# Performance work log

Measured on AMD Instinct MI355X. Metric: run time of the kernel, lower is better.

The kernel has to match this reference:

```python
import jax, jax.numpy as jnp
import numpy as np

B = 4; IN_CH = 256; HEAD_CH = 64; NUM_CLS = 3; H = 128; W = 128
NH = 4; KEY = 16; VAL = 16; OUT_CH = 2
VX = 0.1 * 8; VY = 0.1 * 8  # voxel_size[:2] * out_size_factor
DW = 1.6; DL = 3.9; STRIDE = 1
C_CTR = (HEAD_CH + 2 + NUM_CLS) * 9      # 621
C_COR = (HEAD_CH + 2 + NUM_CLS * 4) * 8  # 624
C_FG = (HEAD_CH + 2 + NUM_CLS) * 9       # 621


def _sampler_points():
    offs = np.arange(-STRIDE, STRIDE + 1, STRIDE, dtype=np.float32)
    oy, ox = np.meshgrid(offs, offs, indexing='ij')
    ctr = np.stack([ox, oy], 0).reshape(2, 9)  # pixel offsets
    cx = np.array([-DW/2, -DW/2, DW/2, DW/2, DL/2, -DL/2, DL/2, -DL/2], np.float32) / VX
    cy = np.array([DL/2, -DL/2, DL/2, -DL/2, -DW/2, -DW/2, DW/2, DW/2], np.float32) / VY
    # faithful to torch: stack(dim=1) -> [8,2] then .view(2,8) (row-major reinterpret)
    cor = np.stack([cx, cy], 1).reshape(2, 8)
    r = max(DW, DL)
    fx = np.array([-r/3, -r/3, -r/3, 0, 0, 0, r/3, r/3, r/3], np.float32) / VX
    fy = np.array([-r/3, 0, r/3, -r/3, 0, r/3, -r/3, 0, r/3], np.float32) / VY
    fg = np.stack([fx, fy], 1).reshape(2, 9)
    return jnp.asarray(ctr), jnp.asarray(cor), jnp.asarray(fg)


def _raw_grid():
    gx = jnp.arange(W, dtype=jnp.float32) + 0.5
    gy = jnp.arange(H, dtype=jnp.float32) + 0.5
    return jnp.stack([jnp.broadcast_to(gx[None, :], (H, W)),
                      jnp.broadcast_to(gy[:, None], (H, W))], 0)  # [2,H,W]


def _conv3x3(x, w, b):
    y = jax.lax.conv_general_dilated(x, w, (1, 1), 'SAME',
                                     dimension_numbers=('NCHW', 'OIHW', 'NCHW'))
    return y + b[None, :, None, None]


def _cbr3(x, w, b, s, t):  # conv3x3 + inference-mode BN (folded scale/shift) + relu
    return jax.nn.relu(_conv3x3(x, w, b) * s[None, :, None, None] + t[None, :, None, None])


def _cbr1(x, w, b, s, t):  # per-head 1x1 conv + BN + relu, w: [NH,O,C], x: [B,C,H,W]
    y = jnp.einsum('noc,bchw->nbohw', w, x) + b[:, None, :, None, None]
    return jax.nn.relu(y * s[:, None, :, None, None] + t[:, None, :, None, None])


def _sample(feats, grids):
    # feats [B,C,H,W]; grids [2,n,H,W] pixel coords. Matches F.grid_sample
    # (bilinear, zeros padding, align_corners=False): sample at pixel coord g-0.5.
    n = grids.shape[1]
    geo = jnp.stack([grids[0] / W, grids[1] / H], 0)  # recover_coords, [2,n,H,W]
    gx, gy = grids[0] - 0.5, grids[1] - 0.5
    x0f = jnp.floor(gx); y0f = jnp.floor(gy)
    dx, dy = gx - x0f, gy - y0f
    x0 = x0f.astype(jnp.int32); y0 = y0f.astype(jnp.int32)
    flat = feats.reshape(B, -1, H * W)

    def gather(xc, yc, wgt):
        valid = ((xc >= 0) & (xc < W) & (yc >= 0) & (yc < H)).astype(feats.dtype) * wgt
        idx = jnp.clip(yc, 0, H - 1) * W + jnp.clip(xc, 0, W - 1)
        v = jnp.take(flat, idx.reshape(-1), axis=2).reshape(B, -1, n, H, W)
        return v * valid[None, None]

    s = (gather(x0, y0, (1 - dx) * (1 - dy)) + gather(x0 + 1, y0, dx * (1 - dy))
         + gather(x0, y0 + 1, (1 - dx) * dy) + gather(x0 + 1, y0 + 1, dx * dy))
    geo_b = jnp.broadcast_to(geo[None], (B,) + geo.shape)
    out = jnp.concatenate([s, geo_b], axis=1)  # [B,C+2,n,H,W]
    return out.reshape(B, -1, H, W)           # channel index = c*n + p, as torch .view


def _forward(base_feats, cc_w, cc_b, cc_s, cc_t, ch_w, ch_b,
             oc_w, oc_b, oc_s, oc_t, oh_w, oh_b,
             fc_w, fc_b, fc_s, fc_t, fh_w, fh_b,
             q_w, q_b, q_s, q_t,
             ck_w, ck_b, ck_s, ck_t, cv_w, cv_b, cv_s, cv_t,
             kk_w, kk_b, kk_s, kk_t, kv_w, kv_b, kv_s, kv_t,
             fk_w, fk_b, fk_s, fk_t, fv_w, fv_b, fv_s, fv_t,
             p1_w, p1_b, p1_s, p1_t, p2_w, p2_b):
    center_feat = _cbr3(base_feats, cc_w, cc_b, cc_s, cc_t)
    center_map = _conv3x3(center_feat, ch_w, ch_b)
    corner_feat = _cbr3(base_feats, oc_w, oc_b, oc_s, oc_t)
    corner_map = _conv3x3(corner_feat, oh_w, oh_b)
    fg_feat = _cbr3(base_feats, fc_w, fc_b, fc_s, fc_t)
    fg_map = _conv3x3(fg_feat, fh_w, fh_b)

    ctr_pts, cor_pts, fg_pts = _sampler_points()
    raw = _raw_grid()
    g_ctr = raw[:, None] + ctr_pts[:, :, None, None]  # [2,9,H,W]
    g_cor = raw[:, None] + cor_pts[:, :, None, None]  # [2,8,H,W]
    g_fg = raw[:, None] + fg_pts[:, :, None, None]    # [2,9,H,W]

    cs = _sample(jnp.concatenate([center_feat, center_map], 1), g_ctr)  # [B,621,H,W]
    os_ = _sample(jnp.concatenate([corner_feat, corner_map], 1), g_cor)  # [B,624,H,W]
    fs = _sample(jnp.concatenate([fg_feat, fg_map], 1), g_fg)            # [B,621,H,W]

    q = _cbr1(base_feats, q_w, q_b, q_s, q_t)  # [NH,B,KEY,H,W]
    ck = _cbr1(cs, ck_w, ck_b, ck_s, ck_t); cv = _cbr1(cs, cv_w, cv_b, cv_s, cv_t)
    ok = _cbr1(os_, kk_w, kk_b, kk_s, kk_t); ov = _cbr1(os_, kv_w, kv_b, kv_s, kv_t)
    fk = _cbr1(fs, fk_w, fk_b, fk_s, fk_t); fv = _cbr1(fs, fv_w, fv_b, fv_s, fv_t)

    logits = jnp.stack([(q * ck).sum(2), (q * ok).sum(2), (q * fk).sum(2)], axis=2)  # [NH,B,3,H,W]
    attw = jax.nn.softmax(logits, axis=2)
    vals = jnp.stack([cv, ov, fv], axis=2)          # [NH,B,3,VAL,H,W]
    att = (attw[:, :, :, None] * vals).sum(2)       # [NH,B,VAL,H,W]

    # predict: 1x1 conv over cat([base_feats, att]) + BN + relu, then 1x1 to out_ch
    h1 = (jnp.einsum('noc,bchw->nbohw', p1_w[:, :, :IN_CH], base_feats)
          + jnp.einsum('nov,nbvhw->nbohw', p1_w[:, :, IN_CH:], att)
          + p1_b[:, None, :, None, None])
    h1 = jax.nn.relu(h1 * p1_s[:, None, :, None, None] + p1_t[:, None, :, None, None])
    pred = jnp.einsum('npo,nbohw->nbphw', p2_w, h1) + p2_b[:, None, :, None, None]
    heads = jnp.moveaxis(pred, 0, 1).reshape(B, NH * OUT_CH, H, W)
    return jnp.concatenate([center_map, corner_map, fg_map, heads], axis=1)  # [B,26,H,W]


def setup_inputs() -> dict:
    ks = iter(jax.random.split(jax.random.key(0), 80))

    def rn(shape, s=0.05):
        return jax.random.normal(next(ks), shape, jnp.float32) * s

    d = {"base_feats": jax.random.normal(next(ks), (B, IN_CH, H, W), jnp.float32)}
    for conv, head, hc in (("cc", "ch", NUM_CLS), ("oc", "oh", NUM_CLS * 4), ("fc", "fh", NUM_CLS)):
        d[conv + "_w"] = rn((HEAD_CH, IN_CH, 3, 3)); d[conv + "_b"] = rn((HEAD_CH,))
        d[conv + "_s"] = 1.0 + rn((HEAD_CH,)); d[conv + "_t"] = rn((HEAD_CH,))
        d[head + "_w"] = rn((hc, HEAD_CH, 3, 3)); d[head + "_b"] = jnp.full((hc,), -2.19, jnp.float32)
    d["q_w"] = rn((NH, KEY, IN_CH)); d["q_b"] = rn((NH, KEY))
    d["q_s"] = 1.0 + rn((NH, KEY)); d["q_t"] = rn((NH, KEY))
    for name, cin, cout in (("ck", C_CTR, KEY), ("cv", C_CTR, VAL), ("kk", C_COR, KEY),
                            ("kv", C_COR, VAL), ("fk", C_FG, KEY), ("fv", C_FG, VAL)):
        d[name + "_w"] = rn((NH, cout, cin)); d[name + "_b"] = rn((NH, cout))
        d[name + "_s"] = 1.0 + rn((NH, cout)); d[name + "_t"] = rn((NH, cout))
    d["p1_w"] = rn((NH, HEAD_CH, IN_CH + VAL)); d["p1_b"] = rn((NH, HEAD_CH))
    d["p1_s"] = 1.0 + rn((NH, HEAD_CH)); d["p1_t"] = rn((NH, HEAD_CH))
    d["p2_w"] = rn((NH, OUT_CH, HEAD_CH)); d["p2_b"] = jnp.full((NH, OUT_CH), -2.19, jnp.float32)
    return d


def reference(base_feats, cc_w, cc_b, cc_s, cc_t, ch_w, ch_b,
              oc_w, oc_b, oc_s, oc_t, oh_w, oh_b,
              fc_w, fc_b, fc_s, fc_t, fh_w, fh_b,
              q_w, q_b, q_s, q_t,
              ck_w, ck_b, ck_s, ck_t, cv_w, cv_b, cv_s, cv_t,
              kk_w, kk_b, kk_s, kk_t, kv_w, kv_b, kv_s, kv_t,
              fk_w, fk_b, fk_s, fk_t, fv_w, fv_b, fv_s, fv_t,
              p1_w, p1_b, p1_s, p1_t, p2_w, p2_b):
    return _forward(base_feats, cc_w, cc_b, cc_s, cc_t, ch_w, ch_b,
                    oc_w, oc_b, oc_s, oc_t, oh_w, oh_b,
                    fc_w, fc_b, fc_s, fc_t, fh_w, fh_b,
                    q_w, q_b, q_s, q_t,
                    ck_w, ck_b, ck_s, ck_t, cv_w, cv_b, cv_s, cv_t,
                    kk_w, kk_b, kk_s, kk_t, kv_w, kv_b, kv_s, kv_t,
                    fk_w, fk_b, fk_s, fk_t, fv_w, fv_b, fv_s, fv_t,
                    p1_w, p1_b, p1_s, p1_t, p2_w, p2_b)
```

## Files before the change

kernel.cpp:

```cpp
#include <hip/hip_runtime.h>
#include <hip/hip_bf16.h>
#include <math.h>


#define HW 16384
#define WIMG 128

typedef unsigned short ushortT;
typedef __attribute__((ext_vector_type(8))) short short8;
typedef __attribute__((ext_vector_type(4))) float floatx4;
typedef __attribute__((ext_vector_type(4))) unsigned uintx4;

constexpr size_t OFF_KV    = 16777216;
constexpr size_t OFF_A16   = 29360128;
constexpr size_t OFF_B16   = 38012928;
constexpr size_t OFF_CWT   = 46057216;
constexpr size_t OFF_CB    = OFF_CWT + 442368;
constexpr size_t OFF_HWT   = OFF_CB + 192;
constexpr size_t OFF_QWT   = OFF_HWT + 20736;
constexpr size_t OFF_QB    = OFF_QWT + 16384;
constexpr size_t OFF_KVW   = OFF_QB + 64;
constexpr size_t OFF_GEO   = OFF_KVW + 241664;
constexpr size_t OFF_P1WT  = OFF_GEO + 1152;
constexpr size_t OFF_P1B   = OFF_P1WT + 81920;

struct P53 { const float* p[53]; };

__device__ inline ushortT f2bf(float f) {
    unsigned u = __float_as_uint(f);
    unsigned r = (u + 0x7FFFu + ((u >> 16) & 1u)) >> 16;
    return (ushortT)r;
}
__device__ inline unsigned packbf(float a, float b) {
    return (unsigned)f2bf(a) | ((unsigned)f2bf(b) << 16);
}
__device__ inline float bf2f(ushortT u) {
    return __uint_as_float((unsigned)u << 16);
}

typedef __attribute__((address_space(3))) ushortT lds_us;
typedef __attribute__((address_space(1))) const ushortT glb_us;
__device__ inline void gload_lds16(const ushortT* g, ushortT* ldsbase) {
    __builtin_amdgcn_global_load_lds((glb_us*)g, (lds_us*)ldsbase, 16, 0, 0);
}

__device__ const float c_ox[3][9] = {
    {-1.f, 0.f, 1.f, -1.f, 0.f, 1.f, -1.f, 0.f, 1.f},
    {-1.f, 2.4375f, -1.f, -2.4375f, 1.f, 2.4375f, 1.f, -2.4375f, 0.f},
    {-1.625f, -1.625f, -1.625f, 0.f, -1.625f, 1.625f, 0.f, -1.625f, 0.f}};
__device__ const float c_oy[3][9] = {
    {-1.f, -1.f, -1.f, 0.f, 0.f, 0.f, 1.f, 1.f, 1.f},
    {2.4375f, -1.f, -2.4375f, -1.f, 2.4375f, 1.f, -2.4375f, 1.f, 0.f},
    {0.f, 0.f, 1.625f, 1.625f, -1.625f, 1.625f, 0.f, 1.625f, 1.625f}};

__device__ const int tapX_cor[16] = {-1,-1, 2, 3,-1,-1,-3,-2, 1, 1, 2, 3, 1, 1,-3,-2};
__device__ const int tapY_cor[16] = { 2, 3,-1,-1,-3,-2,-1,-1, 2, 3, 1, 1,-3,-2, 1, 1};
__device__ const int tapR_cor[16] = { 4, 5, 2, 2, 0, 1, 2, 2, 4, 5, 3, 3, 0, 1, 3, 3};

__device__ inline float cornw(float off, int X) {
    float f = floorf(off);
    float d = off - f;
    int fi = (int)f;
    return (X == fi) ? (1.f - d) : (X == fi + 1) ? d : 0.f;
}

__global__ __launch_bounds__(256) void setup_kernel(P53 ptrs, float* __restrict__ ws,
                                                    const float* __restrict__ base,
                                                    ushortT* __restrict__ a16,
                                                    ushortT* __restrict__ b16) {
    int i = blockIdx.x * 256 + threadIdx.x;
    const float* const* p = ptrs.p;
    if (i < 1053312) {
        if (i < 442368) {
            int tap = i / 49152, r = i % 49152;
            int g = r / 1536, r2 = r % 1536;
            int M = r2 >> 3, j = r2 & 7;
            int br = M >> 6, oc = M & 63, ic = g * 8 + j;
            float v = p[1 + 6 * br][(oc * 256 + ic) * 9 + tap] * p[3 + 6 * br][oc];
            ((ushortT*)(ws + OFF_CWT))[i] = f2bf(v);
            return;
        }
        i -= 442368;
        if (i < 192) {
            int br = i >> 6, oc = i & 63;
            ws[OFF_CB + i] = p[2 + 6 * br][oc] * p[3 + 6 * br][oc] + p[4 + 6 * br][oc];
            return;
        }
        i -= 192;
        if (i < 27648) {
            int j = i & 7, m = (i >> 3) & 15, u = (i >> 7) % 72, br = i / 9216;
            int cnt = (br == 1) ? 12 : 3;
            int t = u >> 3, g = u & 7, ic = g * 8 + j;
            const float* hw = (br == 0) ? p[5] : (br == 1) ? p[11] : p[17];
            float v = (m < cnt) ? hw[(m * 64 + ic) * 9 + t] : 0.f;
            ((ushortT*)(ws + OFF_HWT))[i] = f2bf(v);
            return;
        }
        i -= 27648;
        if (i < 16384) {
            int j = i & 7, m = (i >> 3) & 63, sg = i >> 9;
            int k = (sg >> 2) * 32 + (sg & 3) * 8 + j;
            ((ushortT*)(ws + OFF_QWT))[i] = f2bf(p[19][m * 256 + k] * p[21][m]);
            return;
        }
        i -= 16384;
        if (i < 64) { ws[OFF_QB + i] = p[20][i] * p[21][i] + p[22][i]; return; }
        i -= 64;
        if (i < 483328) {
            int j = i & 7, m = (i >> 3) & 127, ug = i >> 10;
            int br, NG, NT, n, C, chb, ul;
            if (ug < 84)       { br = 0; NG = 9; NT = 9;  n = 9; C = 67; chb = 0;  ul = ug; }
            else if (ug < 164) { br = 1; NG = 5; NT = 16; n = 8; C = 76; chb = 0;  ul = ug - 84; }
            else if (ug < 244) { br = 1; NG = 5; NT = 16; n = 8; C = 76; chb = 40; ul = ug - 164; }
            else               { br = 2; NG = 9; NT = 25; n = 9; C = 67; chb = 0;  ul = ug - 244; }
            int t = ul / NG, g = ul % NG;
            int c = chb + g * 8 + j;
            float v = 0.f;
            if (t < NT && c < C) {
                int X, Y;
                if (br == 0)      { X = t % 3 - 1; Y = t / 3 - 1; }
                else if (br == 1) { X = tapX_cor[t]; Y = tapY_cor[t]; }
                else              { X = t % 5 - 2; Y = t / 5 - 2; }
                const float* wsrc = (m < 64) ? p[23 + 8 * br] : p[27 + 8 * br];
                int mo = (m < 64) ? m : m - 64;
                float sc = (m < 64) ? p[25 + 8 * br][mo] : p[29 + 8 * br][mo];
                int Cn = (C + 2) * n;
                float s = 0.f;
                for (int pp = 0; pp < n; ++pp) {
                    float ww = cornw(c_ox[br][pp], X) * cornw(c_oy[br][pp], Y);
                    if (ww != 0.f) s += ww * wsrc[mo * Cn + c * n + pp];
                }
                v = s * sc;
            }
            ((ushortT*)(ws + OFF_KVW))[i] = f2bf(v);
            return;
        }
        i -= 483328;
        if (i < 1152) {
            int br = i / 384, rem = i % 384, which = rem >> 7, m = rem & 127;
            int n = (br == 1) ? 8 : 9, C = (br == 1) ? 76 : 67, Cn = (C + 2) * n;
            const float* wsrc = (m < 64) ? p[23 + 8 * br] : p[27 + 8 * br];
            int mo = (m < 64) ? m : m - 64;
            float sc = (m < 64) ? p[25 + 8 * br][mo] : p[29 + 8 * br][mo];
            float bb = (m < 64) ? p[24 + 8 * br][mo] : p[28 + 8 * br][mo];
            float tt = (m < 64) ? p[26 + 8 * br][mo] : p[30 + 8 * br][mo];
            float v = 0.f;
            if (which == 0) {
                for (int pp = 0; pp < n; ++pp) v += wsrc[mo * Cn + C * n + pp];
                v *= sc;
            } else if (which == 1) {
                for (int pp = 0; pp < n; ++pp) v += wsrc[mo * Cn + (C + 1) * n + pp];
                v *= sc;
            } else {
                for (int pp = 0; pp < n; ++pp)
                    v += wsrc[mo * Cn + C * n + pp] * c_ox[br][pp]
                       + wsrc[mo * Cn + (C + 1) * n + pp] * c_oy[br][pp];
                v = v * sc * 0.0078125f + bb * sc + tt;
            }
            ws[OFF_GEO + br * 384 + which * 128 + m] = v;
            return;
        }
        i -= 1152;
        if (i < 81920) {
            int j = i & 7, M = (i >> 3) & 255, sg = i >> 11;
            int k = (sg >> 2) * 32 + (sg & 3) * 8 + j;
            int nh = M >> 6, oc = M & 63;
            float sc = p[49][nh * 64 + oc];
            float v;
            if (k < 256) v = p[47][(nh * 64 + oc) * 272 + k] * sc;
            else {
                int k2 = k - 256, nh2 = k2 >> 4, va = k2 & 15;
                v = (nh2 == nh) ? p[47][(nh * 64 + oc) * 272 + 256 + va] * sc : 0.f;
            }
            ((ushortT*)(ws + OFF_P1WT))[i] = f2bf(v);
            return;
        }
        i -= 81920;
        if (i < 256) { ws[OFF_P1B + i] = p[48][i] * p[49][i] + p[50][i]; }
        return;
    }
    int idx = i - 1053312;
    if (idx < 4 * 32 * 130 * 130) {
        int col = idx % 130, t = idx / 130;
        int row = t % 130; t /= 130;
        int icg = t & 31, b = t >> 5;
        int h = row - 1, w = col - 1;
        unsigned wds[4] = {0u, 0u, 0u, 0u};
        if ((unsigned)h < 128u && (unsigned)w < 128u) {
            const float* s = base + (size_t)(b * 256 + icg * 8) * HW + h * WIMG + w;
            #pragma unroll
            for (int jp = 0; jp < 4; ++jp)
                wds[jp] = packbf(s[(size_t)(2 * jp) * HW], s[(size_t)(2 * jp + 1) * HW]);
        }
        unsigned* d = (unsigned*)(a16 + (size_t)idx * 8);
        d[0] = wds[0]; d[1] = wds[1]; d[2] = wds[2]; d[3] = wds[3];
        return;
    }
    idx -= 4 * 32 * 130 * 130;
    if (idx < 4 * 28 * 134 * 134) {
        int col = idx % 134, row = (idx / 134) % 134;
        if (row < 3 || row >= 131 || col < 3 || col >= 131) {
            unsigned* d = (unsigned*)(b16 + (size_t)idx * 8);
            d[0] = 0u; d[1] = 0u; d[2] = 0u; d[3] = 0u;
        }
    }
}

__global__ __launch_bounds__(256) void conv_base_mfma(
    const ushortT* __restrict__ a16, const ushortT* __restrict__ wA,
    const float* __restrict__ cb, ushortT* __restrict__ b16)
{
    const int wv = threadIdx.x >> 6, lane = threadIdx.x & 63;
    const int sub = lane >> 4, ln = lane & 15;
    const int xh = blockIdx.x, h = blockIdx.y, b = blockIdx.z;
    const int x0 = xh * 64;
    __shared__ __align__(16) ushortT sbuf[2][792 * 8];

    floatx4 acc[3][4];
    #pragma unroll
    for (int mt = 0; mt < 3; ++mt)
        #pragma unroll
        for (int nt = 0; nt < 4; ++nt)
            #pragma unroll
            for (int r = 0; r < 4; ++r) acc[mt][nt][r] = 0.f;

    const int wbase = threadIdx.x & ~63;
    auto stage = [&](int s, int buf) {
        #pragma unroll
        for (int it = 0; it < 4; ++it) {
            int idx = threadIdx.x + it * 256;
            if (idx < 792) {
                int col = idx % 66, t2 = idx / 66;
                int r = t2 % 3, icg = t2 / 3;
                const ushortT* g = a16 +
                    (((size_t)(b * 32 + s * 4 + icg) * 130 + (h + r)) * 130 + (x0 + col)) * 8;
                gload_lds16(g, &sbuf[buf][(size_t)(it * 256 + wbase) * 8]);
            }
        }
    };
    stage(0, 0);
    for (int s = 0; s < 8; ++s) {
        __syncthreads();
        if (s < 7) stage(s + 1, (s + 1) & 1);
        const ushortT* sb = sbuf[s & 1];
        #pragma unroll
        for (int tap = 0; tap < 9; ++tap) {
            const int ky = tap / 3, kx = tap % 3;
            short8 Bf[4];
            #pragma unroll
            for (int nt = 0; nt < 4; ++nt) {
                int c = nt * 16 + ln + kx;
                Bf[nt] = *(const short8*)(sb + ((sub * 3 + ky) * 66 + c) * 8);
            }
            const int g = s * 4 + sub;
            short8 Af[3];
            #pragma unroll
            for (int mt = 0; mt < 3; ++mt) {
                int m = wv * 48 + mt * 16 + ln;
                Af[mt] = *(const short8*)(wA + (((size_t)tap * 32 + g) * 192 + m) * 8);
            }
            #pragma unroll
            for (int mt = 0; mt < 3; ++mt)
                #pragma unroll
                for (int nt = 0; nt < 4; ++nt)
                    acc[mt][nt] = __builtin_amdgcn_mfma_f32_16x16x32_bf16(
                        Af[mt], Bf[nt], acc[mt][nt], 0, 0, 0);
        }
    }
    #pragma unroll
    for (int mt = 0; mt < 3; ++mt) {
        int ocq = wv * 48 + mt * 16 + sub * 4;
        #pragma unroll
        for (int nt = 0; nt < 4; ++nt) {
            int px = x0 + nt * 16 + ln;
            float v0 = fmaxf(acc[mt][nt][0] + cb[ocq + 0], 0.f);
            float v1 = fmaxf(acc[mt][nt][1] + cb[ocq + 1], 0.f);
            float v2 = fmaxf(acc[mt][nt][2] + cb[ocq + 2], 0.f);
            float v3 = fmaxf(acc[mt][nt][3] + cb[ocq + 3], 0.f);
            unsigned lo = packbf(v0, v1), hi = packbf(v2, v3);
            unsigned plo = (unsigned)__shfl_down((int)lo, 16);
            unsigned phi = (unsigned)__shfl_down((int)hi, 16);
            if (!(sub & 1)) {
                int br = ocq >> 6, oc = ocq & 63;
                int grp = ((br == 0) ? 0 : (br == 1) ? 9 : 19) + (oc >> 3);
                uintx4 w = {lo, hi, plo, phi};
                *(uintx4*)(b16 +
                    (((size_t)(b * 28 + grp) * 134 + (h + 3)) * 134 + (px + 3)) * 8) = w;
            }
        }
    }
}

__global__ __launch_bounds__(256) void conv_head_mfma(
    const ushortT* __restrict__ b16c, const ushortT* __restrict__ wH,
    const float* __restrict__ chb, const float* __restrict__ ohb,
    const float* __restrict__ fhb, float* __restrict__ out,
    ushortT* __restrict__ b16)
{
    const int wv = threadIdx.x >> 6, lane = threadIdx.x & 63;
    const int sub = lane >> 4, ln = lane & 15;
    const int h = blockIdx.x;
    const int br = blockIdx.y % 3, b = blockIdx.y / 3;
    const int cnt = (br == 1) ? 12 : 3;
    const int mapb = (br == 0) ? 0 : (br == 1) ? 3 : 15;
    const int grpb = (br == 0) ? 0 : (br == 1) ? 9 : 19;
    const float* bias = (br == 0) ? chb : (br == 1) ? ohb : fhb;
    __shared__ __align__(16) ushortT sbuf[8 * 3 * 130 * 8];
    const int wbase = threadIdx.x & ~63;

    for (int it = 0; it < 13; ++it) {
        int idx = threadIdx.x + it * 256;
        if (idx < 3120) {
            int col = idx % 130, t2 = idx / 130;
            int r = t2 % 3, g = t2 / 3;
            const ushortT* gp = b16c +
                (((size_t)(b * 28 + grpb + g) * 134 + (h + r + 2)) * 134 + (col + 2)) * 8;
            gload_lds16(gp, sbuf + (size_t)(it * 256 + wbase) * 8);
        }
    }
    __syncthreads();

    floatx4 acc[2];
    #pragma unroll
    for (int nt = 0; nt < 2; ++nt)
        #pragma unroll
        for (int r = 0; r < 4; ++r) acc[nt][r] = 0.f;
    #pragma unroll
    for (int k = 0; k < 18; ++k) {
        int u = k * 4 + sub;
        int t = u >> 3, g = u & 7;
        int dxv = t % 3 - 1, ry = t / 3;
        short8 Af = *(const short8*)(wH + ((size_t)(br * 72 + u) * 16 + ln) * 8);
        #pragma unroll
        for (int nt = 0; nt < 2; ++nt) {
            int c = wv * 32 + nt * 16 + ln + dxv + 1;
            short8 Bf = *(const short8*)(sbuf + ((g * 3 + ry) * 130 + c) * 8);
            acc[nt] = __builtin_amdgcn_mfma_f32_16x16x32_bf16(Af, Bf, acc[nt], 0, 0, 0);
        }
    }
    #pragma unroll
    for (int nt = 0; nt < 2; ++nt) {
        int px = wv * 32 + nt * 16 + ln;
        #pragma unroll
        for (int r = 0; r < 4; ++r) {
            int m = sub * 4 + r;
            if (m < cnt) {
                float v = acc[nt][r] + bias[m];
                out[((size_t)b * 26 + mapb + m) * HW + h * WIMG + px] = v;
                int grp = grpb + 8 + (m >> 3), j = m & 7;
                b16[(((size_t)(b * 28 + grp) * 134 + (h + 3)) * 134 + (px + 3)) * 8 + j]
                    = f2bf(v);
            }
        }
    }
}

__global__ __launch_bounds__(256) void kv_all(
    const ushortT* __restrict__ b16, const ushortT* __restrict__ kvw,
    const float* __restrict__ geob, ushortT* __restrict__ kvout)
{
    const int lane = threadIdx.x & 63, wv = threadIdx.x >> 6;
    const int sub = lane >> 4, ln = lane & 15;
    const int mw = wv >> 1, nw = wv & 1;
    const int x0 = blockIdx.x * 64, h = blockIdx.y;
    const int brv = blockIdx.z >> 2, b = blockIdx.z & 3;

    const int NGRP = (brv == 1) ? 5 : 9;
    const int NTAP = (brv == 0) ? 9 : (brv == 1) ? 16 : 25;
    const int ROWS = (brv == 0) ? 3 : (brv == 1) ? 6 : 5;
    const int COLS = (brv == 0) ? 66 : (brv == 1) ? 70 : 68;
    const int XMIN = (brv == 0) ? -1 : (brv == 1) ? -3 : -2;
    const int NCHUNK = (brv == 0) ? 21 : (brv == 1) ? 20 : 57;
    const int NPH = (brv == 1) ? 2 : 1;
    const int UBASE = (brv == 0) ? 0 : (brv == 1) ? 9 : 19;
    const ushortT* wU0 = kvw + ((brv == 0) ? 0 : (brv == 1) ? 86016 : 249856);
    const float* geo = geob + brv * 384;

    __shared__ __align__(16) ushortT sbuf[3060 * 8];
    __shared__ int lut[232];
    const int wbase = threadIdx.x & ~63;
    const int thrB = (nw * 32 + ln) * 16;

    if (threadIdx.x < 4 * NCHUNK) {
        int u = threadIdx.x;
        unsigned Mng = 0xFFFFFFFFu / (unsigned)NGRP + 1u;
        int t = (int)__umulhi((unsigned)u, Mng);
        int g = u - t * NGRP;
        if (t >= NTAP) t = 0;
        int dxv, ry;
        if (brv == 0)      { dxv = t % 3 - 1; ry = t / 3; }
        else if (brv == 1) { dxv = tapX_cor[t]; ry = tapR_cor[t]; }
        else               { dxv = t % 5 - 2; ry = t / 5; }
        lut[u] = ((g * ROWS + ry) * COLS + (dxv - XMIN)) * 16;
    }

    floatx4 acc[4][2];
    #pragma unroll
    for (int mt = 0; mt < 4; ++mt)
        #pragma unroll
        for (int nt = 0; nt < 2; ++nt)
            #pragma unroll
            for (int r = 0; r < 4; ++r) acc[mt][nt][r] = 0.f;

    const unsigned Mcols = 0xFFFFFFFFu / (unsigned)COLS + 1u;
    const unsigned Mrows = 0xFFFFFFFFu / (unsigned)ROWS + 1u;
    const int NELEM = NGRP * ROWS * COLS;
    const int NITER = (NELEM + 255) >> 8;

    for (int ph = 0; ph < NPH; ++ph) {
        const ushortT* wU = wU0 + (size_t)ph * (NCHUNK * 4 * 1024);
        const ushortT* wp0 = wU + (size_t)sub * 1024 + (mw * 64 + ln) * 8;
        __syncthreads();
        for (int it = 0; it < NITER; ++it) {
            int idx = threadIdx.x + it * 256;
            if (idx < NELEM) {
                int row = (int)__umulhi((unsigned)idx, Mcols);
                int col = idx - row * COLS;
                int grp = (int)__umulhi((unsigned)row, Mrows);
                int rw = row - grp * ROWS;
                int dy = (ROWS == 6) ? ((rw < 3) ? rw - 3 : rw - 2) : (rw - (ROWS >> 1));
                const ushortT* gp = b16 +
                    (((size_t)(b * 28 + UBASE + ph * NGRP + grp) * 134 + (h + dy + 3)) * 134
                     + (x0 + col + XMIN + 3)) * 8;
                gload_lds16(gp, sbuf + (size_t)(it * 256 + wbase) * 8);
            }
        }
        __syncthreads();

        const char* sb8 = (const char*)sbuf;
        short8 A0[4], B0[2], A1[4], B1[2];
        auto ldf = [&](int k, short8 A[4], short8 B[2]) {
            const ushortT* wp = wp0 + (size_t)k * 4096;
            #pragma unroll
            for (int mt = 0; mt < 4; ++mt)
                A[mt] = *(const short8*)(wp + mt * 128);
            int bb = lut[k * 4 + sub] + thrB;
            #pragma unroll
            for (int nt = 0; nt < 2; ++nt)
                B[nt] = *(const short8*)(sb8 + bb + nt * 256);
        };
        auto dom = [&](short8 A[4], short8 B[2]) {
            #pragma unroll
            for (int mt = 0; mt < 4; ++mt)
                #pragma unroll
                for (int nt = 0; nt < 2; ++nt)
                    acc[mt][nt] = __builtin_amdgcn_mfma_f32_16x16x32_bf16(
                        A[mt], B[nt], acc[mt][nt], 0, 0, 0);
        };
        ldf(0, A0, B0);
        for (int k = 0; k < NCHUNK; k += 2) {
            bool h1 = (k + 1 < NCHUNK);
            if (h1) ldf(k + 1, A1, B1);
            dom(A0, B0);
            if (k + 2 < NCHUNK) ldf(k + 2, A0, B0);
            if (h1) dom(A1, B1);
        }
    }

    const float fy = (h + 0.5f) * 0.0078125f;
    #pragma unroll
    for (int mt = 0; mt < 4; ++mt)
        #pragma unroll
        for (int nt = 0; nt < 2; ++nt) {
            int px = x0 + nw * 32 + nt * 16 + ln;
            float fx = (px + 0.5f) * 0.0078125f;
            #pragma unroll
            for (int r = 0; r < 4; ++r) {
                int Mi = mw * 64 + mt * 16 + sub * 4 + r;
                float v = acc[mt][nt][r] + geo[Mi] * fx + geo[128 + Mi] * fy + geo[256 + Mi];
                kvout[((size_t)(brv * 4 + b) * 128 + Mi) * HW + h * WIMG + px] =
                    f2bf(fmaxf(v, 0.f));
            }
        }
}

__global__ __launch_bounds__(256) void attn_pred_mfma(
    float* __restrict__ ws, const float* __restrict__ p2w,
    const float* __restrict__ p2b, float* __restrict__ out)
{
    const int wv = threadIdx.x >> 6, lane = threadIdx.x & 63;
    const int sub = lane >> 4, ln = lane & 15;
    const int px0 = blockIdx.x * 64, b = blockIdx.y;
    const ushortT* wP1 = (const ushortT*)(ws + OFF_P1WT);
    const ushortT* wQ  = (const ushortT*)(ws + OFF_QWT);
    const ushortT* a16 = (const ushortT*)(ws + OFF_A16);
    const ushortT* kv = (const ushortT*)(ws + OFF_KV);
    const float* p1b = ws + OFF_P1B;
    const float* qb  = ws + OFF_QB;
    __shared__ __align__(16) ushortT xbuf[40 * 64 * 8];
    __shared__ __align__(16) ushortT qld[64 * 64];

    const int mypx = threadIdx.x & 63, nh = threadIdx.x >> 6;
    const int gpx = px0 + mypx, hh = gpx >> 7, ww = gpx & 127;
    #pragma unroll
    for (int g2 = 0; g2 < 8; ++g2) {
        int g = nh * 8 + g2;
        const ushortT* gp = a16 +
            (((size_t)(b * 32 + g) * 130 + (hh + 1)) * 130 + (ww + 1)) * 8;
        gload_lds16(gp, xbuf + (size_t)g * 64 * 8);
    }
    __syncthreads();

    {
        floatx4 qacc[4];
        #pragma unroll
        for (int nt = 0; nt < 4; ++nt)
            #pragma unroll
            for (int r = 0; r < 4; ++r) qacc[nt][r] = 0.f;
        #pragma unroll
        for (int kk = 0; kk < 8; ++kk) {
            short8 Af = *(const short8*)(wQ + (((kk * 4 + sub) * 64) + wv * 16 + ln) * 8);
            #pragma unroll
            for (int nt = 0; nt < 4; ++nt) {
                short8 Bf = *(const short8*)(xbuf + (((kk * 4 + sub) * 64) + nt * 16 + ln) * 8);
                qacc[nt] = __builtin_amdgcn_mfma_f32_16x16x32_bf16(Af, Bf, qacc[nt], 0, 0, 0);
            }
        }
        #pragma unroll
        for (int nt = 0; nt < 4; ++nt)
            #pragma unroll
            for (int r = 0; r < 4; ++r) {
                int row = wv * 16 + sub * 4 + r;
                qld[row * 64 + nt * 16 + ln] = f2bf(fmaxf(qacc[nt][r] + qb[row], 0.f));
            }
    }
    __syncthreads();

    {
        float l[3];
        #pragma unroll
        for (int br = 0; br < 3; ++br) {
            float s = 0.f;
            #pragma unroll
            for (int ko = 0; ko < 16; ++ko)
                s = fmaf(bf2f(qld[(nh * 16 + ko) * 64 + mypx]),
                         bf2f(kv[(size_t)((br * 4 + b) * 128 + nh * 16 + ko) * HW + gpx]), s);
            l[br] = s;
        }
        float m = fmaxf(l[0], fmaxf(l[1], l[2]));
        float e0 = __expf(l[0] - m), e1 = __expf(l[1] - m), e2 = __expf(l[2] - m);
        float inv = 1.f / (e0 + e1 + e2);
        float aw0 = e0 * inv, aw1 = e1 * inv, aw2 = e2 * inv;
        #pragma unroll
        for (int vap = 0; vap < 8; ++vap) {
            int va0 = vap * 2, va1 = vap * 2 + 1;
            float a0 =
                aw0 * bf2f(kv[(size_t)((0 * 4 + b) * 128 + 64 + nh * 16 + va0) * HW + gpx]) +
                aw1 * bf2f(kv[(size_t)((1 * 4 + b) * 128 + 64 + nh * 16 + va0) * HW + gpx]) +
                aw2 * bf2f(kv[(size_t)((2 * 4 + b) * 128 + 64 + nh * 16 + va0) * HW + gpx]);
            float a1 =
                aw0 * bf2f(kv[(size_t)((0 * 4 + b) * 128 + 64 + nh * 16 + va1) * HW + gpx]) +
                aw1 * bf2f(kv[(size_t)((1 * 4 + b) * 128 + 64 + nh * 16 + va1) * HW + gpx]) +
                aw2 * bf2f(kv[(size_t)((2 * 4 + b) * 128 + 64 + nh * 16 + va1) * HW + gpx]);
            int g = 32 + nh * 2 + (vap >> 2), wo = vap & 3;
            ((unsigned*)xbuf)[(g * 64 + mypx) * 4 + wo] = packbf(a0, a1);
        }
    }
    __syncthreads();

    floatx4 acc[4][4];
    #pragma unroll
    for (int mt = 0; mt < 4; ++mt)
        #pragma unroll
        for (int nt = 0; nt < 4; ++nt)
            #pragma unroll
            for (int r = 0; r < 4; ++r) acc[mt][nt][r] = 0.f;
    #pragma unroll
    for (int kk = 0; kk < 10; ++kk) {
        short8 Bf[4];
        #pragma unroll
        for (int nt = 0; nt < 4; ++nt)
            Bf[nt] = *(const short8*)(xbuf + (((kk * 4 + sub) * 64) + nt * 16 + ln) * 8);
        #pragma unroll
        for (int mt = 0; mt < 4; ++mt) {
            short8 Af = *(const short8*)(wP1 +
                (((size_t)(kk * 4 + sub) * 256) + wv * 64 + mt * 16 + ln) * 8);
            #pragma unroll
            for (int nt = 0; nt < 4; ++nt)
                acc[mt][nt] = __builtin_amdgcn_mfma_f32_16x16x32_bf16(Af, Bf[nt], acc[mt][nt], 0, 0, 0);
        }
    }

    float po0[4] = {0.f, 0.f, 0.f, 0.f}, po1[4] = {0.f, 0.f, 0.f, 0.f};
    #pragma unroll
    for (int mt = 0; mt < 4; ++mt)
        #pragma unroll
        for (int r = 0; r < 4; ++r) {
            int oc = mt * 16 + sub * 4 + r;
            float bias = p1b[wv * 64 + oc];
            float w0 = p2w[(wv * 2 + 0) * 64 + oc];
            float w1 = p2w[(wv * 2 + 1) * 64 + oc];
            #pragma unroll
            for (int nt = 0; nt < 4; ++nt) {
                float hv = fmaxf(acc[mt][nt][r] + bias, 0.f);
                po0[nt] = fmaf(w0, hv, po0[nt]);
                po1[nt] = fmaf(w1, hv, po1[nt]);
            }
        }
    #pragma unroll
    for (int nt = 0; nt < 4; ++nt) {
        po0[nt] += __shfl_xor(po0[nt], 16);
        po0[nt] += __shfl_xor(po0[nt], 32);
        po1[nt] += __shfl_xor(po1[nt], 16);
        po1[nt] += __shfl_xor(po1[nt], 32);
    }
    if (sub == 0) {
        #pragma unroll
        for (int nt = 0; nt < 4; ++nt) {
            int px = px0 + nt * 16 + ln;
            out[((size_t)b * 26 + 18 + wv * 2 + 0) * HW + px] = po0[nt] + p2b[wv * 2 + 0];
            out[((size_t)b * 26 + 18 + wv * 2 + 1) * HW + px] = po1[nt] + p2b[wv * 2 + 1];
        }
    }
}

extern "C" void kernel_launch(void* const* d_in, const int* in_sizes, int n_in,
                              void* d_out, int out_size, void* d_ws, size_t ws_size,
                              hipStream_t stream) {
    (void)in_sizes; (void)n_in; (void)out_size; (void)ws_size;
    float* ws  = (float*)d_ws;
    float* out = (float*)d_out;
    const float* base = (const float*)d_in[0];
    P53 ptrs;
    for (int i = 0; i < 53; ++i) ptrs.p[i] = (const float*)d_in[i];

    ushortT* a16 = (ushortT*)(ws + OFF_A16);
    ushortT* b16 = (ushortT*)(ws + OFF_B16);
    ushortT* kvb = (ushortT*)(ws + OFF_KV);

    setup_kernel<<<20421, 256, 0, stream>>>(ptrs, ws, base, a16, b16);
    conv_base_mfma<<<dim3(2, 128, 4), 256, 0, stream>>>(
        a16, (const ushortT*)(ws + OFF_CWT), ws + OFF_CB, b16);
    conv_head_mfma<<<dim3(128, 12), 256, 0, stream>>>(
        b16, (const ushortT*)(ws + OFF_HWT),
        (const float*)d_in[6], (const float*)d_in[12], (const float*)d_in[18],
        out, b16);
    kv_all<<<dim3(2, 128, 12), 256, 0, stream>>>(
        b16, (const ushortT*)(ws + OFF_KVW), ws + OFF_GEO, kvb);
    attn_pred_mfma<<<dim3(256, 4), 256, 0, stream>>>(ws, (const float*)d_in[51],
                                                     (const float*)d_in[52], out);
}
```

Measured before the change: 434.7 us.

## Split KV conv into per-branch templated kernels with double-buffered group staging

The single runtime-branched kv_all kernel becomes a templated kv_grp<BRV> launched once per branch. Branch constants are now compile-time, and the LUT is replaced by per-lane register offsets. Input channels are processed one 8-channel group at a time through two LDS buffers, so the next group's global-to-LDS load overlaps the current group's MFMAs. The KV weights are re-laid out per group in setup, and the workspace offsets are tightened to bf16 sizes. This trades one large LDS tile per block for a smaller one to allow higher occupancy (launch bounds 256,6), at the cost of a barrier per group and three kernel launches instead of one.

```diff
diff --git a/kernel.cpp b/kernel.cpp
--- a/kernel.cpp
+++ b/kernel.cpp
@@ -15,14 +15,14 @@
 constexpr size_t OFF_A16   = 29360128;
 constexpr size_t OFF_B16   = 38012928;
 constexpr size_t OFF_CWT   = 46057216;
-constexpr size_t OFF_CB    = OFF_CWT + 442368;
+constexpr size_t OFF_CB    = OFF_CWT + 221184;
 constexpr size_t OFF_HWT   = OFF_CB + 192;
-constexpr size_t OFF_QWT   = OFF_HWT + 20736;
-constexpr size_t OFF_QB    = OFF_QWT + 16384;
+constexpr size_t OFF_QWT   = OFF_HWT + 13824;
+constexpr size_t OFF_QB    = OFF_QWT + 8192;
 constexpr size_t OFF_KVW   = OFF_QB + 64;
-constexpr size_t OFF_GEO   = OFF_KVW + 241664;
+constexpr size_t OFF_GEO   = OFF_KVW + 266240;
 constexpr size_t OFF_P1WT  = OFF_GEO + 1152;
-constexpr size_t OFF_P1B   = OFF_P1WT + 81920;
+constexpr size_t OFF_P1B   = OFF_P1WT + 40960;
 
 struct P53 { const float* p[53]; };
 
@@ -70,7 +70,7 @@
                                                     ushortT* __restrict__ b16) {
     int i = blockIdx.x * 256 + threadIdx.x;
     const float* const* p = ptrs.p;
-    if (i < 1053312) {
+    if (i < 1102464) {
         if (i < 442368) {
             int tap = i / 49152, r = i % 49152;
             int g = r / 1536, r2 = r % 1536;
@@ -106,17 +106,18 @@
         i -= 16384;
         if (i < 64) { ws[OFF_QB + i] = p[20][i] * p[21][i] + p[22][i]; return; }
         i -= 64;
-        if (i < 483328) {
-            int j = i & 7, m = (i >> 3) & 127, ug = i >> 10;
-            int br, NG, NT, n, C, chb, ul;
-            if (ug < 84)       { br = 0; NG = 9; NT = 9;  n = 9; C = 67; chb = 0;  ul = ug; }
-            else if (ug < 164) { br = 1; NG = 5; NT = 16; n = 8; C = 76; chb = 0;  ul = ug - 84; }
-            else if (ug < 244) { br = 1; NG = 5; NT = 16; n = 8; C = 76; chb = 40; ul = ug - 164; }
-            else               { br = 2; NG = 9; NT = 25; n = 9; C = 67; chb = 0;  ul = ug - 244; }
-            int t = ul / NG, g = ul % NG;
-            int c = chb + g * 8 + j;
+        if (i < 532480) {
+            int br, NQ, NTAP, n, C, i2;
+            if (i < 110592)      { br = 0; NQ = 3; NTAP = 9;  n = 9; C = 67; i2 = i; }
+            else if (i < 274432) { br = 1; NQ = 4; NTAP = 16; n = 8; C = 76; i2 = i - 110592; }
+            else                 { br = 2; NQ = 7; NTAP = 25; n = 9; C = 67; i2 = i - 274432; }
+            int gsz = NQ * 4096;
+            int g = i2 / gsz, r = i2 % gsz;
+            int q = r >> 12, r2 = r & 4095;
+            int sub = r2 >> 10, m = (r2 >> 3) & 127, j = r2 & 7;
+            int t = q * 4 + sub, c = g * 8 + j;
             float v = 0.f;
-            if (t < NT && c < C) {
+            if (t < NTAP && c < C) {
                 int X, Y;
                 if (br == 0)      { X = t % 3 - 1; Y = t / 3 - 1; }
                 else if (br == 1) { X = tapX_cor[t]; Y = tapY_cor[t]; }
@@ -135,7 +136,7 @@
             ((ushortT*)(ws + OFF_KVW))[i] = f2bf(v);
             return;
         }
-        i -= 483328;
+        i -= 532480;
         if (i < 1152) {
             int br = i / 384, rem = i % 384, which = rem >> 7, m = rem & 127;
             int n = (br == 1) ? 8 : 9, C = (br == 1) ? 76 : 67, Cn = (C + 2) * n;
@@ -179,7 +180,7 @@
         if (i < 256) { ws[OFF_P1B + i] = p[48][i] * p[49][i] + p[50][i]; }
         return;
     }
-    int idx = i - 1053312;
+    int idx = i - 1102464;
     if (idx < 4 * 32 * 130 * 130) {
         int col = idx % 130, t = idx / 130;
         int row = t % 130; t /= 130;
@@ -355,44 +356,58 @@
     }
 }
 
-__global__ __launch_bounds__(256) void kv_all(
+template<int BRV>
+__global__ __launch_bounds__(256, 6) void kv_grp(
     const ushortT* __restrict__ b16, const ushortT* __restrict__ kvw,
     const float* __restrict__ geob, ushortT* __restrict__ kvout)
 {
+    constexpr int NG    = (BRV == 0) ? 9  : (BRV == 1) ? 10 : 9;
+    constexpr int NTAP  = (BRV == 0) ? 9  : (BRV == 1) ? 16 : 25;
+    constexpr int NQ    = (BRV == 0) ? 3  : (BRV == 1) ? 4  : 7;
+    constexpr int ROWS  = (BRV == 0) ? 3  : (BRV == 1) ? 6  : 5;
+    constexpr int COLS  = (BRV == 0) ? 66 : (BRV == 1) ? 70 : 68;
+    constexpr int XMIN  = (BRV == 0) ? -1 : (BRV == 1) ? -3 : -2;
+    constexpr int UBASE = (BRV == 0) ? 0  : (BRV == 1) ? 9  : 19;
+    constexpr int NEL   = ROWS * COLS;
+    constexpr int NIT   = (NEL + 255) / 256;
+    constexpr int WBASE = (BRV == 0) ? 0 : (BRV == 1) ? 110592 : 274432;
+
     const int lane = threadIdx.x & 63, wv = threadIdx.x >> 6;
     const int sub = lane >> 4, ln = lane & 15;
     const int mw = wv >> 1, nw = wv & 1;
     const int x0 = blockIdx.x * 64, h = blockIdx.y;
-    const int brv = blockIdx.z >> 2, b = blockIdx.z & 3;
-
-    const int NGRP = (brv == 1) ? 5 : 9;
-    const int NTAP = (brv == 0) ? 9 : (brv == 1) ? 16 : 25;
-    const int ROWS = (brv == 0) ? 3 : (brv == 1) ? 6 : 5;
-    const int COLS = (brv == 0) ? 66 : (brv == 1) ? 70 : 68;
-    const int XMIN = (brv == 0) ? -1 : (brv == 1) ? -3 : -2;
-    const int NCHUNK = (brv == 0) ? 21 : (brv == 1) ? 20 : 57;
-    const int NPH = (brv == 1) ? 2 : 1;
-    const int UBASE = (brv == 0) ? 0 : (brv == 1) ? 9 : 19;
-    const ushortT* wU0 = kvw + ((brv == 0) ? 0 : (brv == 1) ? 86016 : 249856);
-    const float* geo = geob + brv * 384;
-
-    __shared__ __align__(16) ushortT sbuf[3060 * 8];
-    __shared__ int lut[232];
+    const int b = blockIdx.z;
+
+    __shared__ __align__(16) ushortT sbuf[2][NEL * 8];
     const int wbase = threadIdx.x & ~63;
     const int thrB = (nw * 32 + ln) * 16;
 
-    if (threadIdx.x < 4 * NCHUNK) {
-        int u = threadIdx.x;
-        unsigned Mng = 0xFFFFFFFFu / (unsigned)NGRP + 1u;
-        int t = (int)__umulhi((unsigned)u, Mng);
-        int g = u - t * NGRP;
-        if (t >= NTAP) t = 0;
+    int boff[NQ];
+    #pragma unroll
+    for (int q = 0; q < NQ; ++q) {
+        int t = q * 4 + sub;
         int dxv, ry;
-        if (brv == 0)      { dxv = t % 3 - 1; ry = t / 3; }
-        else if (brv == 1) { dxv = tapX_cor[t]; ry = tapR_cor[t]; }
-        else               { dxv = t % 5 - 2; ry = t / 5; }
-        lut[u] = ((g * ROWS + ry) * COLS + (dxv - XMIN)) * 16;
-    }
+        if (t >= NTAP)          { dxv = -XMIN; ry = 0; }
+        else if (BRV == 0)      { dxv = t % 3 - 1; ry = t / 3; }
+        else if (BRV == 1)      { dxv = tapX_cor[t]; ry = tapR_cor[t]; }
+        else                    { dxv = t % 5 - 2; ry = t / 5; }
+        boff[q] = (ry * COLS + (dxv - XMIN)) * 16 + thrB;
+    }
+
+    auto stage = [&](int g, int buf) {
+        #pragma unroll
+        for (int it = 0; it < NIT; ++it) {
+            int idx = threadIdx.x + it * 256;
+            if (idx < NEL) {
+                int rw = idx / COLS, col = idx % COLS;
+                int dy = (BRV == 1) ? ((rw < 3) ? rw - 3 : rw - 2) : (rw - ROWS / 2);
+                const ushortT* gp = b16 +
+                    (((size_t)(b * 28 + UBASE + g) * 134 + (h + dy + 3)) * 134
+                     + (x0 + col + XMIN + 3)) * 8;
+                gload_lds16(gp, &sbuf[buf][(size_t)(it * 256 + wbase) * 8]);
+            }
+        }
+    };
 
     floatx4 acc[4][2];
     #pragma unroll
@@ -402,39 +417,21 @@
             #pragma unroll
             for (int r = 0; r < 4; ++r) acc[mt][nt][r] = 0.f;
 
-    const unsigned Mcols = 0xFFFFFFFFu / (unsigned)COLS + 1u;
-    const unsigned Mrows = 0xFFFFFFFFu / (unsigned)ROWS + 1u;
-    const int NELEM = NGRP * ROWS * COLS;
-    const int NITER = (NELEM + 255) >> 8;
-
-    for (int ph = 0; ph < NPH; ++ph) {
-        const ushortT* wU = wU0 + (size_t)ph * (NCHUNK * 4 * 1024);
-        const ushortT* wp0 = wU + (size_t)sub * 1024 + (mw * 64 + ln) * 8;
-        __syncthreads();
-        for (int it = 0; it < NITER; ++it) {
-            int idx = threadIdx.x + it * 256;
-            if (idx < NELEM) {
-                int row = (int)__umulhi((unsigned)idx, Mcols);
-                int col = idx - row * COLS;
-                int grp = (int)__umulhi((unsigned)row, Mrows);
-                int rw = row - grp * ROWS;
-                int dy = (ROWS == 6) ? ((rw < 3) ? rw - 3 : rw - 2) : (rw - (ROWS >> 1));
-                const ushortT* gp = b16 +
-                    (((size_t)(b * 28 + UBASE + ph * NGRP + grp) * 134 + (h + dy + 3)) * 134
-                     + (x0 + col + XMIN + 3)) * 8;
-                gload_lds16(gp, sbuf + (size_t)(it * 256 + wbase) * 8);
-            }
-        }
-        __syncthreads();
-
-        const char* sb8 = (const char*)sbuf;
+    const ushortT* wp0 = kvw + WBASE + (size_t)sub * 1024 + (mw * 64 + ln) * 8;
+
+    stage(0, 0);
+    __syncthreads();
+    int cur = 0;
+    for (int g = 0; g < NG; ++g) {
+        const char* sb8 = (const char*)sbuf[cur];
+        const ushortT* wg = wp0 + (size_t)g * (NQ * 4096);
         short8 A0[4], B0[2], A1[4], B1[2];
-        auto ldf = [&](int k, short8 A[4], short8 B[2]) {
-            const ushortT* wp = wp0 + (size_t)k * 4096;
+        auto ldf = [&](int q, short8 A[4], short8 B[2]) {
+            const ushortT* wp = wg + (size_t)q * 4096;
             #pragma unroll
             for (int mt = 0; mt < 4; ++mt)
                 A[mt] = *(const short8*)(wp + mt * 128);
-            int bb = lut[k * 4 + sub] + thrB;
+            int bb = boff[q];
             #pragma unroll
             for (int nt = 0; nt < 2; ++nt)
                 B[nt] = *(const short8*)(sb8 + bb + nt * 256);
@@ -448,15 +445,20 @@
                         A[mt], B[nt], acc[mt][nt], 0, 0, 0);
         };
         ldf(0, A0, B0);
-        for (int k = 0; k < NCHUNK; k += 2) {
-            bool h1 = (k + 1 < NCHUNK);
-            if (h1) ldf(k + 1, A1, B1);
+        if (g + 1 < NG) stage(g + 1, cur ^ 1);
+        #pragma unroll
+        for (int q = 0; q < NQ; q += 2) {
+            bool h1 = (q + 1 < NQ);
+            if (h1) ldf(q + 1, A1, B1);
             dom(A0, B0);
-            if (k + 2 < NCHUNK) ldf(k + 2, A0, B0);
+            if (q + 2 < NQ) ldf(q + 2, A0, B0);
             if (h1) dom(A1, B1);
         }
-    }
-
+        __syncthreads();
+        cur ^= 1;
+    }
+
+    const float* geo = geob + BRV * 384;
     const float fy = (h + 0.5f) * 0.0078125f;
     #pragma unroll
     for (int mt = 0; mt < 4; ++mt)
@@ -468,7 +470,7 @@
             for (int r = 0; r < 4; ++r) {
                 int Mi = mw * 64 + mt * 16 + sub * 4 + r;
                 float v = acc[mt][nt][r] + geo[Mi] * fx + geo[128 + Mi] * fy + geo[256 + Mi];
-                kvout[((size_t)(brv * 4 + b) * 128 + Mi) * HW + h * WIMG + px] =
+                kvout[((size_t)(BRV * 4 + b) * 128 + Mi) * HW + h * WIMG + px] =
                     f2bf(fmaxf(v, 0.f));
             }
         }
@@ -627,16 +629,18 @@
     ushortT* a16 = (ushortT*)(ws + OFF_A16);
     ushortT* b16 = (ushortT*)(ws + OFF_B16);
     ushortT* kvb = (ushortT*)(ws + OFF_KV);
-
-    setup_kernel<<<20421, 256, 0, stream>>>(ptrs, ws, base, a16, b16);
+    const ushortT* kvw = (const ushortT*)(ws + OFF_KVW);
+
+    setup_kernel<<<20613, 256, 0, stream>>>(ptrs, ws, base, a16, b16);
     conv_base_mfma<<<dim3(2, 128, 4), 256, 0, stream>>>(
         a16, (const ushortT*)(ws + OFF_CWT), ws + OFF_CB, b16);
     conv_head_mfma<<<dim3(128, 12), 256, 0, stream>>>(
         b16, (const ushortT*)(ws + OFF_HWT),
         (const float*)d_in[6], (const float*)d_in[12], (const float*)d_in[18],
         out, b16);
-    kv_all<<<dim3(2, 128, 12), 256, 0, stream>>>(
-        b16, (const ushortT*)(ws + OFF_KVW), ws + OFF_GEO, kvb);
+    kv_grp<0><<<dim3(2, 128, 4), 256, 0, stream>>>(b16, kvw, ws + OFF_GEO, kvb);
+    kv_grp<1><<<dim3(2, 128, 4), 256, 0, stream>>>(b16, kvw, ws + OFF_GEO, kvb);
+    kv_grp<2><<<dim3(2, 128, 4), 256, 0, stream>>>(b16, kvw, ws + OFF_GEO, kvb);
     attn_pred_mfma<<<dim3(256, 4), 256, 0, stream>>>(ws, (const float*)d_in[51],
                                                      (const float*)d_in[52], out);
 }
```

Measured after the change: 460.4 us. 1.06x slower.
